# Kernel optimization log

Measured on AMD Instinct MI355X. Metric: run time of the kernel, lower is better.

## Reference

```python
import jax, jax.numpy as jnp
import numpy as np

B, T, E, A, S, H = 1024, 64, 1024, 10, 30, 200  # batch, time, embed, actdim, stoch, deter==hidden
MIN_STD = 0.1


def _xavier(key, fan_in, fan_out):
    lim = float(np.sqrt(6.0 / (fan_in + fan_out)))
    return jax.random.uniform(key, (fan_in, fan_out), jnp.float32, -lim, lim)


def setup_inputs() -> dict:
    key = jax.random.key(0)
    ks = jax.random.split(key, 20)
    gl = 1.0 / float(np.sqrt(H))  # torch GRUCell default init bound
    inp = {
        'embed': jax.random.normal(ks[0], (B, T, E), jnp.float32),
        'action': jax.random.normal(ks[1], (B, T, A), jnp.float32),
        'eps_post': jax.random.normal(ks[2], (T, B, S), jnp.float32),
        'eps_prior': jax.random.normal(ks[3], (T, B, S), jnp.float32),
        # Linear weights stored [in, out] (transposed vs torch) so x @ W works.
        'img1_w': _xavier(ks[4], A + S, H), 'img1_b': jnp.zeros((H,), jnp.float32),
        'gru_wi': jax.random.uniform(ks[5], (H, 3 * H), jnp.float32, -gl, gl),
        'gru_wh': jax.random.uniform(ks[6], (H, 3 * H), jnp.float32, -gl, gl),
        'gru_bi': jax.random.uniform(ks[7], (3 * H,), jnp.float32, -gl, gl),
        'gru_bh': jax.random.uniform(ks[8], (3 * H,), jnp.float32, -gl, gl),
        'img2_w': _xavier(ks[9], H, H), 'img2_b': jnp.zeros((H,), jnp.float32),
        'img3_w': _xavier(ks[10], H, 2 * S), 'img3_b': jnp.zeros((2 * S,), jnp.float32),
        'obs1_w': _xavier(ks[11], H + E, H), 'obs1_b': jnp.zeros((H,), jnp.float32),
        'obs2_w': _xavier(ks[12], H, 2 * S), 'obs2_b': jnp.zeros((2 * S,), jnp.float32),
    }
    return inp


def _observe(embed, action, eps_post, eps_prior,
             img1_w, img1_b, gru_wi, gru_wh, gru_bi, gru_bh,
             img2_w, img2_b, img3_w, img3_b, obs1_w, obs1_b, obs2_w, obs2_b):
    elu = jax.nn.elu
    embed_t = jnp.transpose(embed, (1, 0, 2))   # [T,B,E]
    action_t = jnp.transpose(action, (1, 0, 2))  # [T,B,A]

    def step(carry, xs):
        stoch, deter = carry
        a, emb, ep_q, ep_p = xs
        # img_step (prior)
        x = elu(jnp.concatenate([stoch, a], -1) @ img1_w + img1_b)
        gi = x @ gru_wi + gru_bi
        gh = deter @ gru_wh + gru_bh
        ir, iz, i_n = jnp.split(gi, 3, axis=-1)
        hr, hz, h_n = jnp.split(gh, 3, axis=-1)
        r = jax.nn.sigmoid(ir + hr)
        z = jax.nn.sigmoid(iz + hz)
        n = jnp.tanh(i_n + r * h_n)
        deter = (1.0 - z) * n + z * deter
        y = elu(deter @ img2_w + img2_b) @ img3_w + img3_b
        p_mean, p_std = jnp.split(y, 2, axis=-1)
        p_std = jax.nn.softplus(p_std) + MIN_STD
        p_stoch = p_mean + p_std * ep_p  # rsample
        # obs_step (posterior)
        o = elu(jnp.concatenate([deter, emb], -1) @ obs1_w + obs1_b) @ obs2_w + obs2_b
        q_mean, q_std = jnp.split(o, 2, axis=-1)
        q_std = jax.nn.softplus(q_std) + MIN_STD
        q_stoch = q_mean + q_std * ep_q  # rsample
        out = jnp.concatenate([q_mean, q_std, q_stoch, deter,
                               p_mean, p_std, p_stoch, deter], axis=-1)
        return (q_stoch, deter), out

    init = (jnp.zeros((B, S), embed.dtype), jnp.zeros((B, H), embed.dtype))
    _, outs = jax.lax.scan(step, init, (action_t, embed_t, eps_post, eps_prior))
    # outs: [T, B, 2*(3S+H)] -> [B, T, 580]; layout: post(mean,std,stoch,deter)|prior(mean,std,stoch,deter)
    return jnp.transpose(outs, (1, 0, 2))


def reference(embed, action, eps_post, eps_prior,
              img1_w, img1_b, gru_wi, gru_wh, gru_bi, gru_bh,
              img2_w, img2_b, img3_w, img3_b, obs1_w, obs1_b, obs2_w, obs2_b):
    return _observe(embed, action, eps_post, eps_prior,
                    img1_w, img1_b, gru_wi, gru_wh, gru_bi, gru_bh,
                    img2_w, img2_b, img3_w, img3_b, obs1_w, obs1_b, obs2_w, obs2_b)
```

## Files before the change

### kernel.cpp

```cpp
#include <hip/hip_runtime.h>

#define T_ 64

typedef __attribute__((ext_vector_type(4))) float f32x4;
typedef __attribute__((ext_vector_type(8))) short s16x8;

__device__ __forceinline__ unsigned short f2bf(float f) {
  unsigned u = __float_as_uint(f);
  u = (u + 0x7FFFu + ((u >> 16) & 1u)) >> 16;
  return (unsigned short)u;
}
__device__ __forceinline__ float bf2f(unsigned short h) {
  return __uint_as_float(((unsigned)h) << 16);
}
__device__ __forceinline__ float eluf(float x) { return x > 0.f ? x : __expf(x) - 1.f; }
__device__ __forceinline__ float sigmf(float x) { return 1.f / (1.f + __expf(-x)); }
__device__ __forceinline__ float tanh_(float x) {
  float xx = fminf(fmaxf(x, -30.f), 30.f);
  float e = __expf(-2.f * xx);
  return (1.f - e) / (1.f + e);
}
__device__ __forceinline__ float softpf(float x) {
  return x > 20.f ? x : __logf(1.f + __expf(x));
}

#define OPW1   0
#define OPWI   6656
#define OPWH   126464
#define OPO1D  246272
#define OPO2   286208
#define OPI2   298496
#define OPI3   345088
#define OWIWT  359424
#define OWHWT  364416
#define OO1DWT 369408
#define OI1WT  371072
#define OO2WT  372736
#define PK_U16 373248

#define OFF_PK  26214400
#define OFF_SWZ 26960896

__device__ void pack_mat(int idx, int stride, const float* __restrict__ W,
                         int K, int N, int KT, int NT, unsigned short* __restrict__ dst) {
  int total = KT * NT * 512;
  for (int i = idx; i < total; i += stride) {
    int j = i & 7, l = (i >> 3) & 63, rem = i >> 9;
    int kt = rem % KT, nt = rem / KT;
    int n = nt * 16 + (l & 15), k = kt * 32 + (l >> 4) * 8 + j;
    float v = (k < K && n < N) ? W[(size_t)k * N + n] : 0.f;
    dst[i] = f2bf(v);
  }
}

__device__ void pack_gate(int idx, int stride, const float* __restrict__ W,
                          unsigned short* __restrict__ dst) {
  int total = 3 * 13 * 6 * 512;
  for (int i = idx; i < total; i += stride) {
    int j = i & 7, l = (i >> 3) & 63, rem = i >> 9;
    int kt = rem % 6, rem2 = rem / 6, nt = rem2 % 13, g = rem2 / 13;
    int u = nt * 16 + (l & 15);
    int k = kt * 32 + (l >> 4) * 8 + j;
    float v = (u < 200) ? W[(size_t)k * 600 + g * 200 + u] : 0.f;
    dst[i] = f2bf(v);
  }
}

__global__ void prep_weights(const float* __restrict__ w1, const float* __restrict__ wi,
                             const float* __restrict__ wh, const float* __restrict__ i2,
                             const float* __restrict__ i3, const float* __restrict__ obs1w,
                             const float* __restrict__ o2,
                             unsigned short* __restrict__ pk,
                             unsigned short* __restrict__ swz) {
  int idx = blockIdx.x * blockDim.x + threadIdx.x;
  int stride = gridDim.x * blockDim.x;
  pack_mat(idx, stride, w1, 40, 200, 1, 13, pk + OPW1);
  pack_gate(idx, stride, wi, pk + OPWI);
  pack_gate(idx, stride, wh, pk + OPWH);
  pack_mat(idx, stride, obs1w, 200, 200, 6, 13, pk + OPO1D);
  pack_mat(idx, stride, o2, 200, 60, 6, 4, pk + OPO2);
  pack_mat(idx, stride, i2, 200, 200, 7, 13, pk + OPI2);
  pack_mat(idx, stride, i3, 200, 60, 7, 4, pk + OPI3);
  for (int i = idx; i < 4992; i += stride) {
    int j = i & 7, c = (i >> 3) % 208, g = i / 1664;
    pk[OWIWT + i] = f2bf((c < 200) ? wi[(size_t)(192 + j) * 600 + g * 200 + c] : 0.f);
    pk[OWHWT + i] = f2bf((c < 200) ? wh[(size_t)(192 + j) * 600 + g * 200 + c] : 0.f);
  }
  for (int i = idx; i < 1664; i += stride) {
    int c = i >> 3, j = i & 7;
    pk[OO1DWT + i] = f2bf((c < 200) ? obs1w[(size_t)(192 + j) * 200 + c] : 0.f);
    pk[OI1WT + i]  = f2bf((c < 200) ? w1[(size_t)(32 + j) * 200 + c] : 0.f);
  }
  for (int i = idx; i < 512; i += stride) {
    int c = i >> 3, j = i & 7;
    pk[OO2WT + i] = f2bf((c < 60) ? o2[(size_t)(192 + j) * 60 + c] : 0.f);
  }
  for (int i = idx; i < 212992; i += stride) {
    int j = i & 7, l = (i >> 3) & 63, rem = i >> 9;
    int nt = rem % 13, kc = rem / 13;
    int k = kc * 32 + ((l >> 4) * 8) + j;
    int n = nt * 16 + (l & 15);
    float v = (n < 200) ? obs1w[(size_t)(200 + k) * 200 + n] : 0.0f;
    swz[i] = f2bf(v);
  }
}

__global__ __launch_bounds__(256) void emb_gemm(const float* __restrict__ embed,
                                                const float* __restrict__ obs1b,
                                                const unsigned short* __restrict__ swz,
                                                unsigned short* __restrict__ emb_pre) {
  __shared__ __align__(16) unsigned short lds_A[64][40];
  int tid = threadIdx.x;
  int lane = tid & 63, w = tid >> 6;
  int R0 = blockIdx.x * 64;
  int tt = R0 >> 10;
  int bb = R0 & 1023;

  f32x4 acc[13];
#pragma unroll
  for (int nt = 0; nt < 13; ++nt) acc[nt] = (f32x4){0.f, 0.f, 0.f, 0.f};

  int i_row = tid >> 2, cg = tid & 3;
  const float* arow = embed + ((size_t)(bb + i_row) * 64 + tt) * 1024 + cg * 8;

  for (int kc = 0; kc < 32; ++kc) {
    __syncthreads();
    {
      const float* p = arow + kc * 32;
      f32x4 a0 = *(const f32x4*)p;
      f32x4 a1 = *(const f32x4*)(p + 4);
      unsigned short* dst = &lds_A[i_row][cg * 8];
      dst[0] = f2bf(a0[0]); dst[1] = f2bf(a0[1]); dst[2] = f2bf(a0[2]); dst[3] = f2bf(a0[3]);
      dst[4] = f2bf(a1[0]); dst[5] = f2bf(a1[1]); dst[6] = f2bf(a1[2]); dst[7] = f2bf(a1[3]);
    }
    __syncthreads();
    s16x8 af = *(const s16x8*)&lds_A[w * 16 + (lane & 15)][(lane >> 4) * 8];
    const unsigned short* bp = swz + (size_t)kc * 6656 + (size_t)lane * 8;
#pragma unroll
    for (int nt = 0; nt < 13; ++nt) {
      s16x8 bfv = *(const s16x8*)(bp + nt * 512);
      acc[nt] = __builtin_amdgcn_mfma_f32_16x16x32_bf16(af, bfv, acc[nt], 0, 0, 0);
    }
  }
  int r0 = R0 + w * 16 + ((lane >> 4) << 2);
  int c0 = lane & 15;
#pragma unroll
  for (int nt = 0; nt < 13; ++nt) {
    int n = nt * 16 + c0;
    if (n < 200) {
      float bv = obs1b[n];
#pragma unroll
      for (int rr = 0; rr < 4; ++rr)
        emb_pre[(size_t)(r0 + rr) * 200 + n] = f2bf(acc[nt][rr] + bv);
    }
  }
}

#define LGKM0  asm volatile("s_waitcnt lgkmcnt(0)" ::: "memory")
#define MEMCLB asm volatile("" ::: "memory")
#define BAR()  __builtin_amdgcn_s_barrier()
#define MFMA16(A, B, C) __builtin_amdgcn_mfma_f32_16x16x32_bf16((A), (B), (C), 0, 0, 0)
#define WV8  asm volatile("s_waitcnt vmcnt(8)" ::: "memory")
#define WV4  asm volatile("s_waitcnt vmcnt(4)" ::: "memory")
#define WV0  asm volatile("s_waitcnt vmcnt(0)" ::: "memory")

typedef __attribute__((address_space(3))) unsigned int u32_lds;
typedef const __attribute__((address_space(1))) unsigned int u32_glb;

__device__ __forceinline__ void gll16(const unsigned short* g, unsigned short* l, int lane) {
  __builtin_amdgcn_global_load_lds((u32_glb*)(g + lane * 8), (u32_lds*)l, 16, 0, 0);
}

template <int TB>
__device__ __forceinline__ f32x4 cons6(const s16x8* A, f32x4 acc,
                                       unsigned short* ringw, const unsigned* toffw,
                                       const unsigned short* pk, int lane) {
#pragma unroll
  for (int kt = 0; kt < 6; ++kt) {
    const int tau = TB + kt;
    if ((tau & 3) == 0) {
      if (tau == 44) { WV0; } else { WV4; }
    }
    s16x8 Bv = *(const s16x8*)(ringw + (tau & 7) * 512 + lane * 8);
    acc = MFMA16(A[kt], Bv, acc);
    if ((tau & 3) == 3) {
      LGKM0; MEMCLB;
#pragma unroll
      for (int k2 = 1; k2 <= 4; ++k2) {
        const int raw = tau + 4 + k2;
        if (raw < 48) gll16(pk + toffw[raw], ringw + (raw & 7) * 512, lane);
      }
      MEMCLB;
    }
  }
  return acc;
}

__device__ __forceinline__ f32x4 res6(const s16x8* A, const s16x8* Wt, f32x4 acc) {
#pragma unroll
  for (int kt = 0; kt < 6; ++kt) acc = MFMA16(A[kt], Wt[kt], acc);
  return acc;
}
__device__ __forceinline__ f32x4 rem1(const s16x8& A6, const unsigned short* wt,
                                      const unsigned short* zb, bool kg0, f32x4 acc) {
  const unsigned short* p = kg0 ? wt : zb;
  return MFMA16(A6, *(const s16x8*)p, acc);
}
__device__ __forceinline__ void grustep(const f32x4& rv, const f32x4& zv,
                                        const f32x4& inv, const f32x4& hnv, f32x4& dv) {
#pragma unroll
  for (int rr = 0; rr < 4; ++rr) {
    float r = sigmf(rv[rr]);
    float z = sigmf(zv[rr]);
    float n = tanh_(inv[rr] + r * hnv[rr]);
    dv[rr] = (1.f - z) * n + z * dv[rr];
  }
}

__global__ __launch_bounds__(512, 1) void scan_v9(
    const float* __restrict__ action, const float* __restrict__ eps_post,
    const float* __restrict__ img1_b, const float* __restrict__ gru_bi,
    const float* __restrict__ gru_bh, const float* __restrict__ obs2_b,
    const unsigned short* __restrict__ pk, const unsigned short* __restrict__ emb_pre,
    float* __restrict__ out) {

  __shared__ __align__(16) unsigned short ring[8][8][512];
  __shared__ __align__(16) unsigned short l_w1[13 * 512];
  __shared__ __align__(16) unsigned short l_wiWT[3][208][8];
  __shared__ __align__(16) unsigned short l_whWT[3][208][8];
  __shared__ __align__(16) unsigned short l_o1dWT[208][8];
  __shared__ __align__(16) unsigned short l_i1WT[208][8];
  __shared__ __align__(16) unsigned short l_o2WT[64][8];
  __shared__ __align__(16) unsigned short zblk[8];
  __shared__ __align__(16) unsigned short xoA[28][16][8];
  __shared__ __align__(16) unsigned short dA[28][16][8];
  __shared__ __align__(16) unsigned short sA[8][16][8];
  __shared__ __align__(16) float s_o[60][20];
  __shared__ __align__(16) float outbuf[16][292];
  __shared__ unsigned l_toff[8][48];

  const int tid = threadIdx.x, lane = tid & 63, w = tid >> 6;
  const int arow = lane & 15, kg = lane >> 4;
  const bool kg0 = (kg == 0);
  const int b0 = blockIdx.x * 16;
  unsigned short* ringw = &ring[w][0][0];
  const unsigned* toffw = &l_toff[w][0];

  for (int i = tid; i < 28 * 16 * 8; i += 512) { (&xoA[0][0][0])[i] = 0; (&dA[0][0][0])[i] = 0; }
  for (int i = tid; i < 8 * 16 * 8; i += 512) (&sA[0][0][0])[i] = 0;
  for (int i = tid; i < 13 * 512; i += 512) l_w1[i] = pk[OPW1 + i];
  for (int i = tid; i < 4992; i += 512) {
    (&l_wiWT[0][0][0])[i] = pk[OWIWT + i];
    (&l_whWT[0][0][0])[i] = pk[OWHWT + i];
  }
  for (int i = tid; i < 1664; i += 512) {
    (&l_o1dWT[0][0])[i] = pk[OO1DWT + i];
    (&l_i1WT[0][0])[i] = pk[OI1WT + i];
  }
  for (int i = tid; i < 512; i += 512) (&l_o2WT[0][0])[i] = pk[OO2WT + i];
  if (tid < 8) zblk[tid] = 0;
  for (int i = tid; i < 8 * 48; i += 512) {
    int ww = i / 48, tau = i % 48;
    unsigned off;
    if (ww < 5) {
      if (tau < 18) { int g = tau / 6, kt = tau % 6; off = OPWI + ((g * 13 + ww) * 6 + kt) * 512; }
      else {
        int t2 = tau - 18, ug = ww + 8;
        if (t2 < 6)       off = OPWI + ((0 * 13 + ug) * 6 + t2) * 512;
        else if (t2 < 12) off = OPWI + ((1 * 13 + ug) * 6 + (t2 - 6)) * 512;
        else if (t2 < 18) off = OPWH + ((1 * 13 + ug) * 6 + (t2 - 12)) * 512;
        else if (t2 < 24) off = OPWI + ((2 * 13 + ug) * 6 + (t2 - 18)) * 512;
        else              off = OPWH + ((2 * 13 + ug) * 6 + (t2 - 24)) * 512;
      }
    } else {
      if (tau < 18) { int g = tau / 6, kt = tau % 6; off = OPWI + ((g * 13 + ww) * 6 + kt) * 512; }
      else if (tau < 42) {
        int i4 = (tau - 18) / 6, kt = (tau - 18) % 6;
        int nt = (ww - 5) * 4 + i4;
        off = OPO1D + (nt * 6 + kt) * 512;
      } else {
        int kt = tau - 42;
        int nt5 = (ww == 5) ? 0 : (ww == 6) ? 1 : 3;
        off = OPO2 + (nt5 * 6 + kt) * 512;
      }
    }
    l_toff[ww][tau] = off;
  }

  s16x8 wB[4][6];
  {
    const unsigned short* base[4];
    if (w < 5) {
      base[0] = pk + OPWH + (size_t)((0 * 13 + w) * 6) * 512;
      base[1] = pk + OPWH + (size_t)((1 * 13 + w) * 6) * 512;
      base[2] = pk + OPWH + (size_t)((2 * 13 + w) * 6) * 512;
      base[3] = pk + OPWH + (size_t)((0 * 13 + w + 8) * 6) * 512;
    } else {
      base[0] = pk + OPWH + (size_t)((0 * 13 + w) * 6) * 512;
      base[1] = pk + OPWH + (size_t)((1 * 13 + w) * 6) * 512;
      base[2] = pk + OPWH + (size_t)((2 * 13 + w) * 6) * 512;
      if (w == 5)      base[3] = pk + OPO1D + (size_t)(12 * 6) * 512;
      else if (w == 7) base[3] = pk + OPO2 + (size_t)(2 * 6) * 512;
      else             base[3] = pk + OPO1D;
    }
#pragma unroll
    for (int s = 0; s < 4; ++s)
#pragma unroll
      for (int kt = 0; kt < 6; ++kt)
        wB[s][kt] = *(const s16x8*)(base[s] + (size_t)kt * 512 + lane * 8);
  }

  const int uA = w * 16 + arow;
  const int uB = (w + 8) * 16 + arow;
  const bool mB = (w < 5) && (uB < 200);
  const int uBc = (uB < 200) ? uB : 199;
  float bsA0 = gru_bi[uA] + gru_bh[uA];
  float bsA1 = gru_bi[200 + uA] + gru_bh[200 + uA];
  float bi2a = gru_bi[400 + uA], bh2a = gru_bh[400 + uA];
  float bsB0 = mB ? (gru_bi[uBc] + gru_bh[uBc]) : 0.f;
  float bsB1 = mB ? (gru_bi[200 + uBc] + gru_bh[200 + uBc]) : 0.f;
  float bi2b = mB ? gru_bi[400 + uBc] : 0.f;
  float bh2b = mB ? gru_bh[400 + uBc] : 0.f;
  float b1A = img1_b[uA];
  float b1B = mB ? img1_b[uBc] : 0.f;
  float b5a = 0.f, b5b = 0.f;
  if (w == 5) b5a = obs2_b[arow];
  else if (w == 6) b5a = obs2_b[16 + arow];
  else if (w == 7) { b5a = (48 + arow < 60) ? obs2_b[48 + arow] : 0.f; b5b = obs2_b[32 + arow]; }

  unsigned short e16[20];
#pragma unroll
  for (int i = 0; i < 20; ++i) e16[i] = 0;
  if (w >= 5) {
#pragma unroll
    for (int i = 0; i < 5; ++i) {
      int nt = (w == 5) ? ((i < 4) ? i : 12) : ((w == 6) ? (4 + ((i < 4) ? i : 3)) : (8 + ((i < 4) ? i : 3)));
      int c = nt * 16 + arow; int cc = (c < 200) ? c : 199;
#pragma unroll
      for (int rr = 0; rr < 4; ++rr)
        e16[i * 4 + rr] = __builtin_nontemporal_load(&emb_pre[((size_t)(b0 + kg * 4 + rr)) * 200 + cc]);
    }
  }
  float epsv;
  { int it = (tid < 480) ? tid : 479;
    epsv = __builtin_nontemporal_load(&eps_post[((size_t)(b0 + it / 30)) * 30 + it % 30]); }
  float act0, actn;
  { int sl = (lane < 20) ? (w * 20 + lane) : (w * 20);
    act0 = __builtin_nontemporal_load(&action[((size_t)(b0 + sl / 10) * T_ + 0) * 10 + sl % 10]);
    actn = __builtin_nontemporal_load(&action[((size_t)(b0 + sl / 10) * T_ + 1) * 10 + sl % 10]); }
  f32x4 dv0 = {0.f, 0.f, 0.f, 0.f}, dv1 = {0.f, 0.f, 0.f, 0.f};

  __syncthreads();
  if (lane < 20) {
    int sl = w * 20 + lane; int kk = sl % 10, r = sl / 10;
    sA[(30 + kk) >> 3][r][(30 + kk) & 7] = f2bf(act0);
  }
#pragma unroll
  for (int tt = 0; tt < 8; ++tt) gll16(pk + toffw[tt], ringw + tt * 512, lane);
  WV0;
  __syncthreads();

  for (int t = 0; t < T_; ++t) {
    {
      s16x8 a0 = *(const s16x8*)&sA[kg][arow][0];
      s16x8 a1 = *(const s16x8*)&sA[4 + kg][arow][0];
      {
        s16x8 B0 = *(const s16x8*)&l_w1[w * 512 + lane * 8];
        f32x4 acc = {b1A, b1A, b1A, b1A};
        acc = MFMA16(a0, B0, acc);
        acc = rem1(a1, &l_i1WT[uA][0], zblk, kg0, acc);
#pragma unroll
        for (int rr = 0; rr < 4; ++rr)
          xoA[uA >> 3][kg * 4 + rr][uA & 7] = f2bf(eluf(acc[rr]));
      }
      if (w < 5) {
        s16x8 B0 = *(const s16x8*)&l_w1[(w + 8) * 512 + lane * 8];
        f32x4 acc = {b1B, b1B, b1B, b1B};
        acc = MFMA16(a0, B0, acc);
        acc = rem1(a1, &l_i1WT[uBc][0], zblk, kg0, acc);
        if (uB < 200) {
#pragma unroll
          for (int rr = 0; rr < 4; ++rr)
            xoA[uB >> 3][kg * 4 + rr][uB & 7] = f2bf(eluf(acc[rr]));
        }
      }
    }
    LGKM0; BAR();

    {
      s16x8 ax[6], ad[6];
#pragma unroll
      for (int kt = 0; kt < 6; ++kt) {
        ax[kt] = *(const s16x8*)&xoA[kt * 4 + kg][arow][0];
        ad[kt] = *(const s16x8*)&dA[kt * 4 + kg][arow][0];
      }
      s16x8 ax6 = *(const s16x8*)&xoA[24 + kg][arow][0];
      s16x8 ad6 = *(const s16x8*)&dA[24 + kg][arow][0];
      if (w < 5) {
        f32x4 rv = cons6<0>(ax, (f32x4){bsA0, bsA0, bsA0, bsA0}, ringw, toffw, pk, lane);
        rv = rem1(ax6, &l_wiWT[0][uA][0], zblk, kg0, rv);
        rv = res6(ad, wB[0], rv);
        rv = rem1(ad6, &l_whWT[0][uA][0], zblk, kg0, rv);
        f32x4 zv = cons6<6>(ax, (f32x4){bsA1, bsA1, bsA1, bsA1}, ringw, toffw, pk, lane);
        zv = rem1(ax6, &l_wiWT[1][uA][0], zblk, kg0, zv);
        zv = res6(ad, wB[1], zv);
        zv = rem1(ad6, &l_whWT[1][uA][0], zblk, kg0, zv);
        f32x4 inv = cons6<12>(ax, (f32x4){bi2a, bi2a, bi2a, bi2a}, ringw, toffw, pk, lane);
        inv = rem1(ax6, &l_wiWT[2][uA][0], zblk, kg0, inv);
        f32x4 hnv = res6(ad, wB[2], (f32x4){bh2a, bh2a, bh2a, bh2a});
        hnv = rem1(ad6, &l_whWT[2][uA][0], zblk, kg0, hnv);
        grustep(rv, zv, inv, hnv, dv0);
#pragma unroll
        for (int rr = 0; rr < 4; ++rr) outbuf[kg * 4 + rr][90 + uA] = dv0[rr];
        f32x4 rv2 = cons6<18>(ax, (f32x4){bsB0, bsB0, bsB0, bsB0}, ringw, toffw, pk, lane);
        rv2 = rem1(ax6, &l_wiWT[0][uBc][0], zblk, kg0, rv2);
        rv2 = res6(ad, wB[3], rv2);
        rv2 = rem1(ad6, &l_whWT[0][uBc][0], zblk, kg0, rv2);
        f32x4 zv2 = cons6<24>(ax, (f32x4){bsB1, bsB1, bsB1, bsB1}, ringw, toffw, pk, lane);
        zv2 = cons6<30>(ad, zv2, ringw, toffw, pk, lane);
        zv2 = rem1(ax6, &l_wiWT[1][uBc][0], zblk, kg0, zv2);
        zv2 = rem1(ad6, &l_whWT[1][uBc][0], zblk, kg0, zv2);
        f32x4 inv2 = cons6<36>(ax, (f32x4){bi2b, bi2b, bi2b, bi2b}, ringw, toffw, pk, lane);
        inv2 = rem1(ax6, &l_wiWT[2][uBc][0], zblk, kg0, inv2);
        f32x4 hnv2 = cons6<42>(ad, (f32x4){bh2b, bh2b, bh2b, bh2b}, ringw, toffw, pk, lane);
        hnv2 = rem1(ad6, &l_whWT[2][uBc][0], zblk, kg0, hnv2);
        grustep(rv2, zv2, inv2, hnv2, dv1);
        if (uB < 200) {
#pragma unroll
          for (int rr = 0; rr < 4; ++rr) outbuf[kg * 4 + rr][90 + uB] = dv1[rr];
        }
      } else {
        f32x4 rv = cons6<0>(ax, (f32x4){bsA0, bsA0, bsA0, bsA0}, ringw, toffw, pk, lane);
        rv = rem1(ax6, &l_wiWT[0][uA][0], zblk, kg0, rv);
        rv = res6(ad, wB[0], rv);
        rv = rem1(ad6, &l_whWT[0][uA][0], zblk, kg0, rv);
        f32x4 zv = cons6<6>(ax, (f32x4){bsA1, bsA1, bsA1, bsA1}, ringw, toffw, pk, lane);
        zv = rem1(ax6, &l_wiWT[1][uA][0], zblk, kg0, zv);
        zv = res6(ad, wB[1], zv);
        zv = rem1(ad6, &l_whWT[1][uA][0], zblk, kg0, zv);
        f32x4 inv = cons6<12>(ax, (f32x4){bi2a, bi2a, bi2a, bi2a}, ringw, toffw, pk, lane);
        inv = rem1(ax6, &l_wiWT[2][uA][0], zblk, kg0, inv);
        f32x4 hnv = res6(ad, wB[2], (f32x4){bh2a, bh2a, bh2a, bh2a});
        hnv = rem1(ad6, &l_whWT[2][uA][0], zblk, kg0, hnv);
        grustep(rv, zv, inv, hnv, dv0);
#pragma unroll
        for (int rr = 0; rr < 4; ++rr) outbuf[kg * 4 + rr][90 + uA] = dv0[rr];
      }
    }
    LGKM0; BAR();

    {
#pragma unroll
      for (int rr = 0; rr < 4; ++rr)
        dA[uA >> 3][kg * 4 + rr][uA & 7] = f2bf(dv0[rr]);
      if (mB) {
#pragma unroll
        for (int rr = 0; rr < 4; ++rr)
          dA[uB >> 3][kg * 4 + rr][uB & 7] = f2bf(dv1[rr]);
      }
    }
    LGKM0; BAR();

    if (w >= 5) {
      s16x8 ad4[6];
#pragma unroll
      for (int kt = 0; kt < 6; ++kt) ad4[kt] = *(const s16x8*)&dA[kt * 4 + kg][arow][0];
      s16x8 ad46 = *(const s16x8*)&dA[24 + kg][arow][0];
      const int ntb = (w - 5) * 4;
      {
        int c = (ntb + 0) * 16 + arow;
        f32x4 acc = cons6<18>(ad4, (f32x4){0.f, 0.f, 0.f, 0.f}, ringw, toffw, pk, lane);
        acc = rem1(ad46, &l_o1dWT[c][0], zblk, kg0, acc);
#pragma unroll
        for (int rr = 0; rr < 4; ++rr)
          xoA[c >> 3][kg * 4 + rr][c & 7] = f2bf(eluf(acc[rr] + bf2f(e16[0 + rr])));
      }
      {
        int c = (ntb + 1) * 16 + arow;
        f32x4 acc = cons6<24>(ad4, (f32x4){0.f, 0.f, 0.f, 0.f}, ringw, toffw, pk, lane);
        acc = rem1(ad46, &l_o1dWT[c][0], zblk, kg0, acc);
#pragma unroll
        for (int rr = 0; rr < 4; ++rr)
          xoA[c >> 3][kg * 4 + rr][c & 7] = f2bf(eluf(acc[rr] + bf2f(e16[4 + rr])));
      }
      {
        int c = (ntb + 2) * 16 + arow;
        f32x4 acc = cons6<30>(ad4, (f32x4){0.f, 0.f, 0.f, 0.f}, ringw, toffw, pk, lane);
        acc = rem1(ad46, &l_o1dWT[c][0], zblk, kg0, acc);
#pragma unroll
        for (int rr = 0; rr < 4; ++rr)
          xoA[c >> 3][kg * 4 + rr][c & 7] = f2bf(eluf(acc[rr] + bf2f(e16[8 + rr])));
      }
      {
        int c = (ntb + 3) * 16 + arow;
        f32x4 acc = cons6<36>(ad4, (f32x4){0.f, 0.f, 0.f, 0.f}, ringw, toffw, pk, lane);
        acc = rem1(ad46, &l_o1dWT[c][0], zblk, kg0, acc);
#pragma unroll
        for (int rr = 0; rr < 4; ++rr)
          xoA[c >> 3][kg * 4 + rr][c & 7] = f2bf(eluf(acc[rr] + bf2f(e16[12 + rr])));
      }
      if (w == 5) {
        int c = 192 + arow;
        f32x4 acc = res6(ad4, wB[3], (f32x4){0.f, 0.f, 0.f, 0.f});
        acc = rem1(ad46, &l_o1dWT[c][0], zblk, kg0, acc);
        if (c < 200) {
#pragma unroll
          for (int rr = 0; rr < 4; ++rr)
            xoA[c >> 3][kg * 4 + rr][c & 7] = f2bf(eluf(acc[rr] + bf2f(e16[16 + rr])));
        }
      }
    }
    LGKM0; BAR();

    if (w >= 5) {
      s16x8 a5[6];
#pragma unroll
      for (int kt = 0; kt < 6; ++kt) a5[kt] = *(const s16x8*)&xoA[kt * 4 + kg][arow][0];
      s16x8 a56 = *(const s16x8*)&xoA[24 + kg][arow][0];
      int c5 = (w == 5) ? arow : (w == 6) ? (16 + arow) : (48 + arow);
      f32x4 acc = cons6<42>(a5, (f32x4){b5a, b5a, b5a, b5a}, ringw, toffw, pk, lane);
      {
        int c5c = (c5 < 64) ? c5 : 63;
        acc = rem1(a56, &l_o2WT[c5c][0], zblk, kg0, acc);
      }
      if (c5 < 60) *(f32x4*)&s_o[c5][kg * 4] = acc;
      if (w == 7) {
        int c5r = 32 + arow;
        f32x4 acc2 = res6(a5, wB[3], (f32x4){b5b, b5b, b5b, b5b});
        acc2 = rem1(a56, &l_o2WT[c5r][0], zblk, kg0, acc2);
        *(f32x4*)&s_o[c5r][kg * 4] = acc2;
      }
    }
    LGKM0; BAR();

    MEMCLB;
    {
      if (tid < 480) {
        int r = tid / 30, j = tid % 30;
        float qm = s_o[j][r];
        float qs = softpf(s_o[j + 30][r]) + 0.1f;
        float qst = qm + qs * epsv;
        outbuf[r][j] = qm; outbuf[r][30 + j] = qs; outbuf[r][60 + j] = qst;
        sA[j >> 3][r][j & 7] = f2bf(qst);
      }
      if (lane < 20) {
        int sl = w * 20 + lane; int kk = sl % 10, r = sl / 10;
        sA[(30 + kk) >> 3][r][(30 + kk) & 7] = f2bf(actn);
      }
      int tc = (t + 1 < T_) ? t + 1 : T_ - 1;
      int ta = (t + 2 < T_) ? t + 2 : T_ - 1;
      MEMCLB;
      if (w >= 5) {
#pragma unroll
        for (int i = 0; i < 5; ++i) {
          int nt = (w == 5) ? ((i < 4) ? i : 12) : ((w == 6) ? (4 + ((i < 4) ? i : 3)) : (8 + ((i < 4) ? i : 3)));
          int c = nt * 16 + arow; int cc = (c < 200) ? c : 199;
#pragma unroll
          for (int rr = 0; rr < 4; ++rr)
            e16[i * 4 + rr] = __builtin_nontemporal_load(
                &emb_pre[((size_t)tc * 1024 + b0 + kg * 4 + rr) * 200 + cc]);
        }
      }
      { int it = (tid < 480) ? tid : 479;
        epsv = __builtin_nontemporal_load(
            &eps_post[((size_t)tc * 1024 + b0 + it / 30) * 30 + it % 30]); }
      { int sl = (lane < 20) ? (w * 20 + lane) : (w * 20);
        actn = __builtin_nontemporal_load(
            &action[((size_t)(b0 + sl / 10) * T_ + ta) * 10 + sl % 10]); }
      MEMCLB;
    }
    LGKM0; BAR();

#pragma unroll
    for (int k2 = 0; k2 < 3; ++k2) {
      int idx = tid + k2 * 512; idx = (idx < 1168) ? idx : 1167;
      int row = idx / 73, ci = idx - row * 73;
      f32x4 v = *(const f32x4*)&outbuf[row][ci * 4];
      __builtin_nontemporal_store(v, (f32x4*)(out + ((size_t)(b0 + row) * T_ + t) * 580 + ci * 4));
    }
    MEMCLB;
#pragma unroll
    for (int tt = 0; tt < 8; ++tt) gll16(pk + toffw[tt], ringw + tt * 512, lane);
    WV8;
    MEMCLB;
  }
}

__global__ __launch_bounds__(256) void post_head(const float* __restrict__ eps_prior,
                                                 const float* __restrict__ img2_b,
                                                 const float* __restrict__ img3_b,
                                                 const unsigned short* __restrict__ pk,
                                                 float* __restrict__ out) {
  __shared__ __align__(16) unsigned short dAp[4][28][16][8];
  __shared__ __align__(16) unsigned short y1p[4][28][16][8];
  __shared__ __align__(16) float s_p[60][68];
  int b = blockIdx.x;
  int tid = threadIdx.x;
  int lane = tid & 63, w = tid >> 6, arow = lane & 15, kg = lane >> 4;

  for (int i = tid; i < 1536; i += 256) {
    int mt = i / 384, rem = i % 384;
    int gidx = 25 + rem / 128, r2 = (rem % 128) / 8, j = rem & 7;
    dAp[mt][gidx][r2][j] = 0;
    y1p[mt][gidx][r2][j] = 0;
  }
  for (int i = tid; i < 12800; i += 256) {
    int row = i / 200, c = i % 200;
    float v = out[((size_t)(b * 64 + row)) * 580 + 90 + c];
    dAp[row >> 4][c >> 3][row & 15][c & 7] = f2bf(v);
  }
  __syncthreads();

  s16x8 ad[7];
#pragma unroll
  for (int kt = 0; kt < 7; ++kt) ad[kt] = *(const s16x8*)&dAp[w][kt * 4 + kg][arow][0];
#pragma unroll
  for (int nt = 0; nt < 13; ++nt) {
    int col = nt * 16 + arow;
    float bv = (col < 200) ? img2_b[col] : 0.f;
    f32x4 acc = {bv, bv, bv, bv};
#pragma unroll
    for (int kt = 0; kt < 7; ++kt) {
      s16x8 Bv = *(const s16x8*)(pk + OPI2 + (size_t)((nt * 7 + kt) * 512) + lane * 8);
      acc = __builtin_amdgcn_mfma_f32_16x16x32_bf16(ad[kt], Bv, acc, 0, 0, 0);
    }
    if (col < 200) {
#pragma unroll
      for (int rr = 0; rr < 4; ++rr)
        y1p[w][col >> 3][kg * 4 + rr][col & 7] = f2bf(eluf(acc[rr]));
    }
  }
  __syncthreads();

  s16x8 ay[7];
#pragma unroll
  for (int kt = 0; kt < 7; ++kt) ay[kt] = *(const s16x8*)&y1p[w][kt * 4 + kg][arow][0];
#pragma unroll
  for (int nt = 0; nt < 4; ++nt) {
    int col = nt * 16 + arow;
    float bv = (col < 60) ? img3_b[col] : 0.f;
    f32x4 acc = {bv, bv, bv, bv};
#pragma unroll
    for (int kt = 0; kt < 7; ++kt) {
      s16x8 Bv = *(const s16x8*)(pk + OPI3 + (size_t)((nt * 7 + kt) * 512) + lane * 8);
      acc = __builtin_amdgcn_mfma_f32_16x16x32_bf16(ay[kt], Bv, acc, 0, 0, 0);
    }
    if (col < 60) {
#pragma unroll
      for (int rr = 0; rr < 4; ++rr) s_p[col][w * 16 + kg * 4 + rr] = acc[rr];
    }
  }
  __syncthreads();

  for (int i = tid; i < 1920; i += 256) {
    int row = i / 30, j = i % 30;
    float pm = s_p[j][row];
    float ps = softpf(s_p[j + 30][row]) + 0.1f;
    float pst = pm + ps * eps_prior[((size_t)row * 1024 + b) * 30 + j];
    size_t ob = ((size_t)b * 64 + row) * 580;
    out[ob + 290 + j] = pm;
    out[ob + 320 + j] = ps;
    out[ob + 350 + j] = pst;
  }
  for (int i = tid; i < 6400; i += 256) {
    int row = i / 100, c2 = i % 100;
    size_t ob = ((size_t)b * 64 + row) * 580;
    *(float2*)&out[ob + 380 + c2 * 2] = *(const float2*)&out[ob + 90 + c2 * 2];
  }
}

extern "C" void kernel_launch(void* const* d_in, const int* in_sizes, int n_in,
                              void* d_out, int out_size, void* d_ws, size_t ws_size,
                              hipStream_t stream) {
  const float* embed    = (const float*)d_in[0];
  const float* action   = (const float*)d_in[1];
  const float* eps_post = (const float*)d_in[2];
  const float* eps_prior= (const float*)d_in[3];
  const float* img1_w   = (const float*)d_in[4];
  const float* img1_b   = (const float*)d_in[5];
  const float* gru_wi   = (const float*)d_in[6];
  const float* gru_wh   = (const float*)d_in[7];
  const float* gru_bi   = (const float*)d_in[8];
  const float* gru_bh   = (const float*)d_in[9];
  const float* img2_w   = (const float*)d_in[10];
  const float* img2_b   = (const float*)d_in[11];
  const float* img3_w   = (const float*)d_in[12];
  const float* img3_b   = (const float*)d_in[13];
  const float* obs1_w   = (const float*)d_in[14];
  const float* obs1_b   = (const float*)d_in[15];
  const float* obs2_w   = (const float*)d_in[16];
  const float* obs2_b   = (const float*)d_in[17];

  char* ws = (char*)d_ws;
  unsigned short* emb_pre = (unsigned short*)ws;
  unsigned short* pkw     = (unsigned short*)(ws + OFF_PK);
  unsigned short* swz     = (unsigned short*)(ws + OFF_SWZ);
  float* outp = (float*)d_out;

  prep_weights<<<256, 256, 0, stream>>>(img1_w, gru_wi, gru_wh, img2_w, img3_w,
                                        obs1_w, obs2_w, pkw, swz);
  emb_gemm<<<1024, 256, 0, stream>>>(embed, obs1_b, swz, emb_pre);
  scan_v9<<<64, 512, 0, stream>>>(action, eps_post, img1_b, gru_bi, gru_bh,
                                  obs2_b, pkw, emb_pre, outp);
  post_head<<<1024, 256, 0, stream>>>(eps_prior, img2_b, img3_b, pkw, outp);
}
```

Before: 1.094 ms.

## Keep more weight tiles in registers, double-buffer deter, drop a barrier per step

```diff
diff --git a/kernel.cpp b/kernel.cpp
--- a/kernel.cpp
+++ b/kernel.cpp
@@ -3,6 +3,7 @@
 #define T_ 64
 
 typedef __attribute__((ext_vector_type(4))) float f32x4;
+typedef __attribute__((ext_vector_type(2))) float f32x2;
 typedef __attribute__((ext_vector_type(8))) short s16x8;
 
 __device__ __forceinline__ unsigned short f2bf(float f) {
@@ -171,28 +172,35 @@
   __builtin_amdgcn_global_load_lds((u32_glb*)(g + lane * 8), (u32_lds*)l, 16, 0, 0);
 }
 
+template <int TAU>
+__device__ __forceinline__ f32x4 smfma(f32x4 acc, const s16x8& a, unsigned short* ringw,
+                                       const unsigned* co, const unsigned short* pk, int lane) {
+  if ((TAU & 3) == 0) {
+    if (TAU == 32) { WV0; } else { WV4; }
+  }
+  s16x8 Bv = *(const s16x8*)(ringw + (TAU % 12) * 512 + lane * 8);
+  acc = MFMA16(a, Bv, acc);
+  if ((TAU & 3) == 3 && TAU <= 27) {
+    MEMCLB;
+#pragma unroll
+    for (int i2 = 0; i2 < 4; ++i2) {
+      const int nt2 = TAU + 5 + i2;
+      gll16(pk + co[nt2 / 6] + (nt2 % 6) * 512, ringw + (nt2 % 12) * 512, lane);
+    }
+    MEMCLB;
+  }
+  return acc;
+}
+
 template <int TB>
-__device__ __forceinline__ f32x4 cons6(const s16x8* A, f32x4 acc,
-                                       unsigned short* ringw, const unsigned* toffw,
-                                       const unsigned short* pk, int lane) {
-#pragma unroll
-  for (int kt = 0; kt < 6; ++kt) {
-    const int tau = TB + kt;
-    if ((tau & 3) == 0) {
-      if (tau == 44) { WV0; } else { WV4; }
-    }
-    s16x8 Bv = *(const s16x8*)(ringw + (tau & 7) * 512 + lane * 8);
-    acc = MFMA16(A[kt], Bv, acc);
-    if ((tau & 3) == 3) {
-      LGKM0; MEMCLB;
-#pragma unroll
-      for (int k2 = 1; k2 <= 4; ++k2) {
-        const int raw = tau + 4 + k2;
-        if (raw < 48) gll16(pk + toffw[raw], ringw + (raw & 7) * 512, lane);
-      }
-      MEMCLB;
-    }
-  }
+__device__ __forceinline__ f32x4 stream6(const s16x8* A, f32x4 acc, unsigned short* ringw,
+                                         const unsigned* co, const unsigned short* pk, int lane) {
+  acc = smfma<TB + 0>(acc, A[0], ringw, co, pk, lane);
+  acc = smfma<TB + 1>(acc, A[1], ringw, co, pk, lane);
+  acc = smfma<TB + 2>(acc, A[2], ringw, co, pk, lane);
+  acc = smfma<TB + 3>(acc, A[3], ringw, co, pk, lane);
+  acc = smfma<TB + 4>(acc, A[4], ringw, co, pk, lane);
+  acc = smfma<TB + 5>(acc, A[5], ringw, co, pk, lane);
   return acc;
 }
 
@@ -217,15 +225,14 @@
   }
 }
 
-__global__ __launch_bounds__(512, 1) void scan_v9(
+__global__ __launch_bounds__(512, 2) void scan_v10(
     const float* __restrict__ action, const float* __restrict__ eps_post,
     const float* __restrict__ img1_b, const float* __restrict__ gru_bi,
     const float* __restrict__ gru_bh, const float* __restrict__ obs2_b,
     const unsigned short* __restrict__ pk, const unsigned short* __restrict__ emb_pre,
     float* __restrict__ out) {
 
-  __shared__ __align__(16) unsigned short ring[8][8][512];
-  __shared__ __align__(16) unsigned short l_w1[13 * 512];
+  __shared__ __align__(16) unsigned short ring[8][12][512];
   __shared__ __align__(16) unsigned short l_wiWT[3][208][8];
   __shared__ __align__(16) unsigned short l_whWT[3][208][8];
   __shared__ __align__(16) unsigned short l_o1dWT[208][8];
@@ -233,22 +240,23 @@
   __shared__ __align__(16) unsigned short l_o2WT[64][8];
   __shared__ __align__(16) unsigned short zblk[8];
   __shared__ __align__(16) unsigned short xoA[28][16][8];
-  __shared__ __align__(16) unsigned short dA[28][16][8];
+  __shared__ __align__(16) unsigned short dAb[2][28][16][8];
   __shared__ __align__(16) unsigned short sA[8][16][8];
   __shared__ __align__(16) float s_o[60][20];
-  __shared__ __align__(16) float outbuf[16][292];
-  __shared__ unsigned l_toff[8][48];
+  __shared__ __align__(16) float outbuf[16][90];
 
   const int tid = threadIdx.x, lane = tid & 63, w = tid >> 6;
   const int arow = lane & 15, kg = lane >> 4;
   const bool kg0 = (kg == 0);
   const int b0 = blockIdx.x * 16;
   unsigned short* ringw = &ring[w][0][0];
-  const unsigned* toffw = &l_toff[w][0];
-
-  for (int i = tid; i < 28 * 16 * 8; i += 512) { (&xoA[0][0][0])[i] = 0; (&dA[0][0][0])[i] = 0; }
+
+  for (int i = tid; i < 28 * 16 * 8; i += 512) {
+    (&xoA[0][0][0])[i] = 0;
+    (&dAb[0][0][0][0])[i] = 0;
+    (&dAb[1][0][0][0])[i] = 0;
+  }
   for (int i = tid; i < 8 * 16 * 8; i += 512) (&sA[0][0][0])[i] = 0;
-  for (int i = tid; i < 13 * 512; i += 512) l_w1[i] = pk[OPW1 + i];
   for (int i = tid; i < 4992; i += 512) {
     (&l_wiWT[0][0][0])[i] = pk[OWIWT + i];
     (&l_whWT[0][0][0])[i] = pk[OWHWT + i];
@@ -259,56 +267,51 @@
   }
   for (int i = tid; i < 512; i += 512) (&l_o2WT[0][0])[i] = pk[OO2WT + i];
   if (tid < 8) zblk[tid] = 0;
-  for (int i = tid; i < 8 * 48; i += 512) {
-    int ww = i / 48, tau = i % 48;
-    unsigned off;
-    if (ww < 5) {
-      if (tau < 18) { int g = tau / 6, kt = tau % 6; off = OPWI + ((g * 13 + ww) * 6 + kt) * 512; }
-      else {
-        int t2 = tau - 18, ug = ww + 8;
-        if (t2 < 6)       off = OPWI + ((0 * 13 + ug) * 6 + t2) * 512;
-        else if (t2 < 12) off = OPWI + ((1 * 13 + ug) * 6 + (t2 - 6)) * 512;
-        else if (t2 < 18) off = OPWH + ((1 * 13 + ug) * 6 + (t2 - 12)) * 512;
-        else if (t2 < 24) off = OPWI + ((2 * 13 + ug) * 6 + (t2 - 18)) * 512;
-        else              off = OPWH + ((2 * 13 + ug) * 6 + (t2 - 24)) * 512;
-      }
+
+  unsigned co[6];
+  if (w < 5) {
+    co[0] = OPWI + (unsigned)(((0 * 13 + w) * 6) * 512);
+    co[1] = OPWI + (unsigned)(((1 * 13 + w) * 6) * 512);
+    co[2] = OPWI + (unsigned)(((2 * 13 + w) * 6) * 512);
+    co[3] = OPWH + (unsigned)(((1 * 13 + w + 8) * 6) * 512);
+    co[4] = OPWI + (unsigned)(((2 * 13 + w + 8) * 6) * 512);
+    co[5] = OPWH + (unsigned)(((2 * 13 + w + 8) * 6) * 512);
+  } else {
+    co[0] = OPWI + (unsigned)(((2 * 13 + w) * 6) * 512);
+    int ntb = (w - 5) * 4;
+#pragma unroll
+    for (int i = 0; i < 4; ++i) co[1 + i] = OPO1D + (unsigned)(((ntb + i) * 6) * 512);
+    int nt5 = (w == 5) ? 0 : (w == 6) ? 1 : 3;
+    co[5] = OPO2 + (unsigned)((nt5 * 6) * 512);
+  }
+#pragma unroll
+  for (int c = 0; c < 6; ++c) co[c] = __builtin_amdgcn_readfirstlane(co[c]);
+
+  s16x8 R[6][6];
+  {
+    const unsigned short* base[6];
+    base[0] = pk + OPWH + (size_t)((0 * 13 + w) * 6) * 512;
+    base[1] = pk + OPWH + (size_t)((1 * 13 + w) * 6) * 512;
+    base[2] = pk + OPWH + (size_t)((2 * 13 + w) * 6) * 512;
+    if (w < 5) {
+      base[3] = pk + OPWH + (size_t)((0 * 13 + w + 8) * 6) * 512;
+      base[4] = pk + OPWI + (size_t)((0 * 13 + w + 8) * 6) * 512;
+      base[5] = pk + OPWI + (size_t)((1 * 13 + w + 8) * 6) * 512;
     } else {
-      if (tau < 18) { int g = tau / 6, kt = tau % 6; off = OPWI + ((g * 13 + ww) * 6 + kt) * 512; }
-      else if (tau < 42) {
-        int i4 = (tau - 18) / 6, kt = (tau - 18) % 6;
-        int nt = (ww - 5) * 4 + i4;
-        off = OPO1D + (nt * 6 + kt) * 512;
-      } else {
-        int kt = tau - 42;
-        int nt5 = (ww == 5) ? 0 : (ww == 6) ? 1 : 3;
-        off = OPO2 + (nt5 * 6 + kt) * 512;
-      }
-    }
-    l_toff[ww][tau] = off;
-  }
-
-  s16x8 wB[4][6];
-  {
-    const unsigned short* base[4];
-    if (w < 5) {
-      base[0] = pk + OPWH + (size_t)((0 * 13 + w) * 6) * 512;
-      base[1] = pk + OPWH + (size_t)((1 * 13 + w) * 6) * 512;
-      base[2] = pk + OPWH + (size_t)((2 * 13 + w) * 6) * 512;
-      base[3] = pk + OPWH + (size_t)((0 * 13 + w + 8) * 6) * 512;
-    } else {
-      base[0] = pk + OPWH + (size_t)((0 * 13 + w) * 6) * 512;
-      base[1] = pk + OPWH + (size_t)((1 * 13 + w) * 6) * 512;
-      base[2] = pk + OPWH + (size_t)((2 * 13 + w) * 6) * 512;
       if (w == 5)      base[3] = pk + OPO1D + (size_t)(12 * 6) * 512;
       else if (w == 7) base[3] = pk + OPO2 + (size_t)(2 * 6) * 512;
       else             base[3] = pk + OPO1D;
-    }
-#pragma unroll
-    for (int s = 0; s < 4; ++s)
+      base[4] = pk + OPWI + (size_t)((0 * 13 + w) * 6) * 512;
+      base[5] = pk + OPWI + (size_t)((1 * 13 + w) * 6) * 512;
+    }
+#pragma unroll
+    for (int s = 0; s < 6; ++s)
 #pragma unroll
       for (int kt = 0; kt < 6; ++kt)
-        wB[s][kt] = *(const s16x8*)(base[s] + (size_t)kt * 512 + lane * 8);
-  }
+        R[s][kt] = *(const s16x8*)(base[s] + (size_t)kt * 512 + lane * 8);
+  }
+  s16x8 w1Ra = *(const s16x8*)(pk + OPW1 + (size_t)(w * 512) + lane * 8);
+  s16x8 w1Rb = *(const s16x8*)(pk + OPW1 + (size_t)(((w < 5) ? (w + 8) : w) * 512) + lane * 8);
 
   const int uA = w * 16 + arow;
   const int uB = (w + 8) * 16 + arow;
@@ -356,27 +359,29 @@
     sA[(30 + kk) >> 3][r][(30 + kk) & 7] = f2bf(act0);
   }
 #pragma unroll
-  for (int tt = 0; tt < 8; ++tt) gll16(pk + toffw[tt], ringw + tt * 512, lane);
+  for (int tt = 0; tt < 8; ++tt)
+    gll16(pk + co[tt / 6] + (tt % 6) * 512, ringw + (tt % 12) * 512, lane);
   WV0;
   __syncthreads();
 
   for (int t = 0; t < T_; ++t) {
+    unsigned short (*dRd)[16][8] = dAb[t & 1];
+    unsigned short (*dWr)[16][8] = dAb[(t & 1) ^ 1];
+
     {
       s16x8 a0 = *(const s16x8*)&sA[kg][arow][0];
       s16x8 a1 = *(const s16x8*)&sA[4 + kg][arow][0];
       {
-        s16x8 B0 = *(const s16x8*)&l_w1[w * 512 + lane * 8];
         f32x4 acc = {b1A, b1A, b1A, b1A};
-        acc = MFMA16(a0, B0, acc);
+        acc = MFMA16(a0, w1Ra, acc);
         acc = rem1(a1, &l_i1WT[uA][0], zblk, kg0, acc);
 #pragma unroll
         for (int rr = 0; rr < 4; ++rr)
           xoA[uA >> 3][kg * 4 + rr][uA & 7] = f2bf(eluf(acc[rr]));
       }
       if (w < 5) {
-        s16x8 B0 = *(const s16x8*)&l_w1[(w + 8) * 512 + lane * 8];
         f32x4 acc = {b1B, b1B, b1B, b1B};
-        acc = MFMA16(a0, B0, acc);
+        acc = MFMA16(a0, w1Rb, acc);
         acc = rem1(a1, &l_i1WT[uBc][0], zblk, kg0, acc);
         if (uB < 200) {
 #pragma unroll
@@ -388,121 +393,112 @@
     LGKM0; BAR();
 
     {
-      s16x8 ax[6], ad[6];
+      s16x8 ax[7], ad[7];
 #pragma unroll
       for (int kt = 0; kt < 6; ++kt) {
         ax[kt] = *(const s16x8*)&xoA[kt * 4 + kg][arow][0];
-        ad[kt] = *(const s16x8*)&dA[kt * 4 + kg][arow][0];
-      }
-      s16x8 ax6 = *(const s16x8*)&xoA[24 + kg][arow][0];
-      s16x8 ad6 = *(const s16x8*)&dA[24 + kg][arow][0];
+        ad[kt] = *(const s16x8*)&dRd[kt * 4 + kg][arow][0];
+      }
+      ax[6] = *(const s16x8*)&xoA[24 + kg][arow][0];
+      ad[6] = *(const s16x8*)&dRd[24 + kg][arow][0];
       if (w < 5) {
-        f32x4 rv = cons6<0>(ax, (f32x4){bsA0, bsA0, bsA0, bsA0}, ringw, toffw, pk, lane);
-        rv = rem1(ax6, &l_wiWT[0][uA][0], zblk, kg0, rv);
-        rv = res6(ad, wB[0], rv);
-        rv = rem1(ad6, &l_whWT[0][uA][0], zblk, kg0, rv);
-        f32x4 zv = cons6<6>(ax, (f32x4){bsA1, bsA1, bsA1, bsA1}, ringw, toffw, pk, lane);
-        zv = rem1(ax6, &l_wiWT[1][uA][0], zblk, kg0, zv);
-        zv = res6(ad, wB[1], zv);
-        zv = rem1(ad6, &l_whWT[1][uA][0], zblk, kg0, zv);
-        f32x4 inv = cons6<12>(ax, (f32x4){bi2a, bi2a, bi2a, bi2a}, ringw, toffw, pk, lane);
-        inv = rem1(ax6, &l_wiWT[2][uA][0], zblk, kg0, inv);
-        f32x4 hnv = res6(ad, wB[2], (f32x4){bh2a, bh2a, bh2a, bh2a});
-        hnv = rem1(ad6, &l_whWT[2][uA][0], zblk, kg0, hnv);
+        f32x4 rv = stream6<0>(ax, (f32x4){bsA0, bsA0, bsA0, bsA0}, ringw, co, pk, lane);
+        rv = rem1(ax[6], &l_wiWT[0][uA][0], zblk, kg0, rv);
+        rv = res6(ad, R[0], rv);
+        rv = rem1(ad[6], &l_whWT[0][uA][0], zblk, kg0, rv);
+        f32x4 zv = stream6<6>(ax, (f32x4){bsA1, bsA1, bsA1, bsA1}, ringw, co, pk, lane);
+        zv = rem1(ax[6], &l_wiWT[1][uA][0], zblk, kg0, zv);
+        zv = res6(ad, R[1], zv);
+        zv = rem1(ad[6], &l_whWT[1][uA][0], zblk, kg0, zv);
+        f32x4 inv = stream6<12>(ax, (f32x4){bi2a, bi2a, bi2a, bi2a}, ringw, co, pk, lane);
+        inv = rem1(ax[6], &l_wiWT[2][uA][0], zblk, kg0, inv);
+        f32x4 hnv = res6(ad, R[2], (f32x4){bh2a, bh2a, bh2a, bh2a});
+        hnv = rem1(ad[6], &l_whWT[2][uA][0], zblk, kg0, hnv);
         grustep(rv, zv, inv, hnv, dv0);
 #pragma unroll
-        for (int rr = 0; rr < 4; ++rr) outbuf[kg * 4 + rr][90 + uA] = dv0[rr];
-        f32x4 rv2 = cons6<18>(ax, (f32x4){bsB0, bsB0, bsB0, bsB0}, ringw, toffw, pk, lane);
-        rv2 = rem1(ax6, &l_wiWT[0][uBc][0], zblk, kg0, rv2);
-        rv2 = res6(ad, wB[3], rv2);
-        rv2 = rem1(ad6, &l_whWT[0][uBc][0], zblk, kg0, rv2);
-        f32x4 zv2 = cons6<24>(ax, (f32x4){bsB1, bsB1, bsB1, bsB1}, ringw, toffw, pk, lane);
-        zv2 = cons6<30>(ad, zv2, ringw, toffw, pk, lane);
-        zv2 = rem1(ax6, &l_wiWT[1][uBc][0], zblk, kg0, zv2);
-        zv2 = rem1(ad6, &l_whWT[1][uBc][0], zblk, kg0, zv2);
-        f32x4 inv2 = cons6<36>(ax, (f32x4){bi2b, bi2b, bi2b, bi2b}, ringw, toffw, pk, lane);
-        inv2 = rem1(ax6, &l_wiWT[2][uBc][0], zblk, kg0, inv2);
-        f32x4 hnv2 = cons6<42>(ad, (f32x4){bh2b, bh2b, bh2b, bh2b}, ringw, toffw, pk, lane);
-        hnv2 = rem1(ad6, &l_whWT[2][uBc][0], zblk, kg0, hnv2);
+        for (int rr = 0; rr < 4; ++rr)
+          dWr[uA >> 3][kg * 4 + rr][uA & 7] = f2bf(dv0[rr]);
+        f32x4 rv2 = res6(ax, R[4], (f32x4){bsB0, bsB0, bsB0, bsB0});
+        rv2 = rem1(ax[6], &l_wiWT[0][uBc][0], zblk, kg0, rv2);
+        rv2 = res6(ad, R[3], rv2);
+        rv2 = rem1(ad[6], &l_whWT[0][uBc][0], zblk, kg0, rv2);
+        f32x4 zv2 = res6(ax, R[5], (f32x4){bsB1, bsB1, bsB1, bsB1});
+        zv2 = rem1(ax[6], &l_wiWT[1][uBc][0], zblk, kg0, zv2);
+        zv2 = stream6<18>(ad, zv2, ringw, co, pk, lane);
+        zv2 = rem1(ad[6], &l_whWT[1][uBc][0], zblk, kg0, zv2);
+        f32x4 inv2 = stream6<24>(ax, (f32x4){bi2b, bi2b, bi2b, bi2b}, ringw, co, pk, lane);
+        inv2 = rem1(ax[6], &l_wiWT[2][uBc][0], zblk, kg0, inv2);
+        f32x4 hnv2 = stream6<30>(ad, (f32x4){bh2b, bh2b, bh2b, bh2b}, ringw, co, pk, lane);
+        hnv2 = rem1(ad[6], &l_whWT[2][uBc][0], zblk, kg0, hnv2);
         grustep(rv2, zv2, inv2, hnv2, dv1);
         if (uB < 200) {
 #pragma unroll
-          for (int rr = 0; rr < 4; ++rr) outbuf[kg * 4 + rr][90 + uB] = dv1[rr];
+          for (int rr = 0; rr < 4; ++rr)
+            dWr[uB >> 3][kg * 4 + rr][uB & 7] = f2bf(dv1[rr]);
         }
       } else {
-        f32x4 rv = cons6<0>(ax, (f32x4){bsA0, bsA0, bsA0, bsA0}, ringw, toffw, pk, lane);
-        rv = rem1(ax6, &l_wiWT[0][uA][0], zblk, kg0, rv);
-        rv = res6(ad, wB[0], rv);
-        rv = rem1(ad6, &l_whWT[0][uA][0], zblk, kg0, rv);
-        f32x4 zv = cons6<6>(ax, (f32x4){bsA1, bsA1, bsA1, bsA1}, ringw, toffw, pk, lane);
-        zv = rem1(ax6, &l_wiWT[1][uA][0], zblk, kg0, zv);
-        zv = res6(ad, wB[1], zv);
-        zv = rem1(ad6, &l_whWT[1][uA][0], zblk, kg0, zv);
-        f32x4 inv = cons6<12>(ax, (f32x4){bi2a, bi2a, bi2a, bi2a}, ringw, toffw, pk, lane);
-        inv = rem1(ax6, &l_wiWT[2][uA][0], zblk, kg0, inv);
-        f32x4 hnv = res6(ad, wB[2], (f32x4){bh2a, bh2a, bh2a, bh2a});
-        hnv = rem1(ad6, &l_whWT[2][uA][0], zblk, kg0, hnv);
+        f32x4 rv = res6(ax, R[4], (f32x4){bsA0, bsA0, bsA0, bsA0});
+        rv = rem1(ax[6], &l_wiWT[0][uA][0], zblk, kg0, rv);
+        rv = res6(ad, R[0], rv);
+        rv = rem1(ad[6], &l_whWT[0][uA][0], zblk, kg0, rv);
+        f32x4 zv = res6(ax, R[5], (f32x4){bsA1, bsA1, bsA1, bsA1});
+        zv = rem1(ax[6], &l_wiWT[1][uA][0], zblk, kg0, zv);
+        zv = res6(ad, R[1], zv);
+        zv = rem1(ad[6], &l_whWT[1][uA][0], zblk, kg0, zv);
+        f32x4 inv = stream6<0>(ax, (f32x4){bi2a, bi2a, bi2a, bi2a}, ringw, co, pk, lane);
+        inv = rem1(ax[6], &l_wiWT[2][uA][0], zblk, kg0, inv);
+        f32x4 hnv = res6(ad, R[2], (f32x4){bh2a, bh2a, bh2a, bh2a});
+        hnv = rem1(ad[6], &l_whWT[2][uA][0], zblk, kg0, hnv);
         grustep(rv, zv, inv, hnv, dv0);
 #pragma unroll
-        for (int rr = 0; rr < 4; ++rr) outbuf[kg * 4 + rr][90 + uA] = dv0[rr];
+        for (int rr = 0; rr < 4; ++rr)
+          dWr[uA >> 3][kg * 4 + rr][uA & 7] = f2bf(dv0[rr]);
       }
     }
     LGKM0; BAR();
 
-    {
-#pragma unroll
-      for (int rr = 0; rr < 4; ++rr)
-        dA[uA >> 3][kg * 4 + rr][uA & 7] = f2bf(dv0[rr]);
-      if (mB) {
-#pragma unroll
-        for (int rr = 0; rr < 4; ++rr)
-          dA[uB >> 3][kg * 4 + rr][uB & 7] = f2bf(dv1[rr]);
-      }
-    }
-    LGKM0; BAR();
-
     if (w >= 5) {
-      s16x8 ad4[6];
-#pragma unroll
-      for (int kt = 0; kt < 6; ++kt) ad4[kt] = *(const s16x8*)&dA[kt * 4 + kg][arow][0];
-      s16x8 ad46 = *(const s16x8*)&dA[24 + kg][arow][0];
+      s16x8 ad4[7];
+#pragma unroll
+      for (int kt = 0; kt < 6; ++kt) ad4[kt] = *(const s16x8*)&dWr[kt * 4 + kg][arow][0];
+      ad4[6] = *(const s16x8*)&dWr[24 + kg][arow][0];
       const int ntb = (w - 5) * 4;
       {
         int c = (ntb + 0) * 16 + arow;
-        f32x4 acc = cons6<18>(ad4, (f32x4){0.f, 0.f, 0.f, 0.f}, ringw, toffw, pk, lane);
-        acc = rem1(ad46, &l_o1dWT[c][0], zblk, kg0, acc);
+        f32x4 acc = stream6<6>(ad4, (f32x4){0.f, 0.f, 0.f, 0.f}, ringw, co, pk, lane);
+        acc = rem1(ad4[6], &l_o1dWT[c][0], zblk, kg0, acc);
 #pragma unroll
         for (int rr = 0; rr < 4; ++rr)
           xoA[c >> 3][kg * 4 + rr][c & 7] = f2bf(eluf(acc[rr] + bf2f(e16[0 + rr])));
       }
       {
         int c = (ntb + 1) * 16 + arow;
-        f32x4 acc = cons6<24>(ad4, (f32x4){0.f, 0.f, 0.f, 0.f}, ringw, toffw, pk, lane);
-        acc = rem1(ad46, &l_o1dWT[c][0], zblk, kg0, acc);
+        f32x4 acc = stream6<12>(ad4, (f32x4){0.f, 0.f, 0.f, 0.f}, ringw, co, pk, lane);
+        acc = rem1(ad4[6], &l_o1dWT[c][0], zblk, kg0, acc);
 #pragma unroll
         for (int rr = 0; rr < 4; ++rr)
           xoA[c >> 3][kg * 4 + rr][c & 7] = f2bf(eluf(acc[rr] + bf2f(e16[4 + rr])));
       }
       {
         int c = (ntb + 2) * 16 + arow;
-        f32x4 acc = cons6<30>(ad4, (f32x4){0.f, 0.f, 0.f, 0.f}, ringw, toffw, pk, lane);
-        acc = rem1(ad46, &l_o1dWT[c][0], zblk, kg0, acc);
+        f32x4 acc = stream6<18>(ad4, (f32x4){0.f, 0.f, 0.f, 0.f}, ringw, co, pk, lane);
+        acc = rem1(ad4[6], &l_o1dWT[c][0], zblk, kg0, acc);
 #pragma unroll
         for (int rr = 0; rr < 4; ++rr)
           xoA[c >> 3][kg * 4 + rr][c & 7] = f2bf(eluf(acc[rr] + bf2f(e16[8 + rr])));
       }
       {
         int c = (ntb + 3) * 16 + arow;
-        f32x4 acc = cons6<36>(ad4, (f32x4){0.f, 0.f, 0.f, 0.f}, ringw, toffw, pk, lane);
-        acc = rem1(ad46, &l_o1dWT[c][0], zblk, kg0, acc);
+        f32x4 acc = stream6<24>(ad4, (f32x4){0.f, 0.f, 0.f, 0.f}, ringw, co, pk, lane);
+        acc = rem1(ad4[6], &l_o1dWT[c][0], zblk, kg0, acc);
 #pragma unroll
         for (int rr = 0; rr < 4; ++rr)
           xoA[c >> 3][kg * 4 + rr][c & 7] = f2bf(eluf(acc[rr] + bf2f(e16[12 + rr])));
       }
       if (w == 5) {
         int c = 192 + arow;
-        f32x4 acc = res6(ad4, wB[3], (f32x4){0.f, 0.f, 0.f, 0.f});
-        acc = rem1(ad46, &l_o1dWT[c][0], zblk, kg0, acc);
+        f32x4 acc = res6(ad4, R[3], (f32x4){0.f, 0.f, 0.f, 0.f});
+        acc = rem1(ad4[6], &l_o1dWT[c][0], zblk, kg0, acc);
         if (c < 200) {
 #pragma unroll
           for (int rr = 0; rr < 4; ++rr)
@@ -513,27 +509,28 @@
     LGKM0; BAR();
 
     if (w >= 5) {
-      s16x8 a5[6];
+      s16x8 a5[7];
 #pragma unroll
       for (int kt = 0; kt < 6; ++kt) a5[kt] = *(const s16x8*)&xoA[kt * 4 + kg][arow][0];
-      s16x8 a56 = *(const s16x8*)&xoA[24 + kg][arow][0];
+      a5[6] = *(const s16x8*)&xoA[24 + kg][arow][0];
       int c5 = (w == 5) ? arow : (w == 6) ? (16 + arow) : (48 + arow);
-      f32x4 acc = cons6<42>(a5, (f32x4){b5a, b5a, b5a, b5a}, ringw, toffw, pk, lane);
+      f32x4 acc = stream6<30>(a5, (f32x4){b5a, b5a, b5a, b5a}, ringw, co, pk, lane);
       {
         int c5c = (c5 < 64) ? c5 : 63;
-        acc = rem1(a56, &l_o2WT[c5c][0], zblk, kg0, acc);
+        acc = rem1(a5[6], &l_o2WT[c5c][0], zblk, kg0, acc);
       }
       if (c5 < 60) *(f32x4*)&s_o[c5][kg * 4] = acc;
       if (w == 7) {
         int c5r = 32 + arow;
-        f32x4 acc2 = res6(a5, wB[3], (f32x4){b5b, b5b, b5b, b5b});
-        acc2 = rem1(a56, &l_o2WT[c5r][0], zblk, kg0, acc2);
+        f32x4 acc2 = res6(a5, R[3], (f32x4){b5b, b5b, b5b, b5b});
+        acc2 = rem1(a5[6], &l_o2WT[c5r][0], zblk, kg0, acc2);
         *(f32x4*)&s_o[c5r][kg * 4] = acc2;
       }
+    } else {
+      WV0;
     }
     LGKM0; BAR();
 
-    MEMCLB;
     {
       if (tid < 480) {
         int r = tid / 30, j = tid % 30;
@@ -549,7 +546,6 @@
       }
       int tc = (t + 1 < T_) ? t + 1 : T_ - 1;
       int ta = (t + 2 < T_) ? t + 2 : T_ - 1;
-      MEMCLB;
       if (w >= 5) {
 #pragma unroll
         for (int i = 0; i < 5; ++i) {
@@ -567,20 +563,30 @@
       { int sl = (lane < 20) ? (w * 20 + lane) : (w * 20);
         actn = __builtin_nontemporal_load(
             &action[((size_t)(b0 + sl / 10) * T_ + ta) * 10 + sl % 10]); }
-      MEMCLB;
     }
     LGKM0; BAR();
 
 #pragma unroll
-    for (int k2 = 0; k2 < 3; ++k2) {
-      int idx = tid + k2 * 512; idx = (idx < 1168) ? idx : 1167;
-      int row = idx / 73, ci = idx - row * 73;
-      f32x4 v = *(const f32x4*)&outbuf[row][ci * 4];
-      __builtin_nontemporal_store(v, (f32x4*)(out + ((size_t)(b0 + row) * T_ + t) * 580 + ci * 4));
+    for (int k2 = 0; k2 < 2; ++k2) {
+      int idx = tid + k2 * 512;
+      if (idx < 720) {
+        int row = idx / 45, ci = idx - row * 45;
+        f32x2 v = *(const f32x2*)&outbuf[row][ci * 2];
+        __builtin_nontemporal_store(v, (f32x2*)(out + ((size_t)(b0 + row) * T_ + t) * 580 + ci * 2));
+      }
+    }
+#pragma unroll
+    for (int rr = 0; rr < 4; ++rr) {
+      __builtin_nontemporal_store(dv0[rr],
+          out + ((size_t)(b0 + kg * 4 + rr) * T_ + t) * 580 + 90 + uA);
+      if (mB)
+        __builtin_nontemporal_store(dv1[rr],
+            out + ((size_t)(b0 + kg * 4 + rr) * T_ + t) * 580 + 90 + uB);
     }
     MEMCLB;
 #pragma unroll
-    for (int tt = 0; tt < 8; ++tt) gll16(pk + toffw[tt], ringw + tt * 512, lane);
+    for (int tt = 0; tt < 8; ++tt)
+      gll16(pk + co[tt / 6] + (tt % 6) * 512, ringw + (tt % 12) * 512, lane);
     WV8;
     MEMCLB;
   }
@@ -700,7 +706,7 @@
   prep_weights<<<256, 256, 0, stream>>>(img1_w, gru_wi, gru_wh, img2_w, img3_w,
                                         obs1_w, obs2_w, pkw, swz);
   emb_gemm<<<1024, 256, 0, stream>>>(embed, obs1_b, swz, emb_pre);
-  scan_v9<<<64, 512, 0, stream>>>(action, eps_post, img1_b, gru_bi, gru_bh,
-                                  obs2_b, pkw, emb_pre, outp);
+  scan_v10<<<64, 512, 0, stream>>>(action, eps_post, img1_b, gru_bi, gru_bh,
+                                   obs2_b, pkw, emb_pre, outp);
   post_head<<<1024, 256, 0, stream>>>(eps_prior, img2_b, img3_b, pkw, outp);
 }
```

After: 1.461 ms. +33.6%, slower.
